# Performance work log

Hardware: AMD Instinct MI355X
Metric: run time of the kernel (lower is better)

## Reference

```python
import jax, jax.numpy as jnp
import numpy as np

N = 4096      # num nodes == input_dim
HID = 1024    # VAE hidden
LAT = 512     # VAE latent
NH = 4        # GAT heads
NHID = 64     # per-head out features
ALPHA = 0.2   # leaky-relu negative slope
NEG_INF = -9e15


def setup_inputs() -> dict:
    key = jax.random.key(0)
    ks = iter(jax.random.split(key, 32))
    def lin(shape):
        return jax.random.normal(next(ks), shape, jnp.float32) / np.float32(np.sqrt(shape[-1]))
    inp = {
        "x": jax.random.uniform(next(ks), (N,), jnp.float32),
        "eps": jax.random.normal(next(ks), (LAT,), jnp.float32),
        "adj": jax.random.uniform(next(ks), (N, N), jnp.float32) < 0.01,  # ~40 nbrs/node
        "enc_w1": lin((HID, N)), "enc_b1": jnp.zeros((HID,), jnp.float32),
        "enc_w2": lin((HID, HID)), "enc_b2": jnp.zeros((HID,), jnp.float32),
        "enc_w3": lin((LAT, HID)), "enc_b3": jnp.zeros((LAT,), jnp.float32),
        "enc_w4": lin((LAT, HID)), "enc_b4": jnp.zeros((LAT,), jnp.float32),
        "dec_w1": lin((HID, LAT)), "dec_b1": jnp.zeros((HID,), jnp.float32),
        "dec_w2": lin((HID, HID)), "dec_b2": jnp.zeros((HID,), jnp.float32),
        "dec_w3": lin((N, HID)), "dec_b3": jnp.zeros((N,), jnp.float32),
        "gat_W": lin((NH, 1, NHID)),
        "gat_a": lin((NH, 2 * NHID, 1)),
        "out_W": lin((NH * NHID, 1)),
        "out_a": lin((2, 1)),
    }
    return inp


def _linear(h, w, b):
    return h @ w.T + b


def reference(x, eps, adj, enc_w1, enc_b1, enc_w2, enc_b2, enc_w3, enc_b3,
              enc_w4, enc_b4, dec_w1, dec_b1, dec_w2, dec_b2, dec_w3, dec_b3,
              gat_W, gat_a, out_W, out_a):
    # ---- VAE encoder ----
    h = jax.nn.relu(_linear(x, enc_w1, enc_b1))
    h = jax.nn.relu(_linear(h, enc_w2, enc_b2))
    mu = _linear(h, enc_w3, enc_b3)
    logvar = _linear(h, enc_w4, enc_b4)
    # ---- reparameterize ----
    z = mu + eps * jnp.exp(0.5 * logvar)
    # ---- VAE decoder ----
    h = jax.nn.relu(_linear(z, dec_w1, dec_b1))
    h = jax.nn.relu(_linear(h, dec_w2, dec_b2))
    x_hat = jax.nn.sigmoid(_linear(h, dec_w3, dec_b3))          # [N]

    # ---- GAT (eval mode: dropout = identity) ----
    def gat_layer(xin, W, a):
        Wh = xin @ W                                             # [N, F]
        f = W.shape[1]
        e = jax.nn.leaky_relu(Wh @ a[:f] + (Wh @ a[f:]).T, ALPHA)  # [N, N]
        e = jnp.where(adj, e, NEG_INF)
        att = jax.nn.softmax(e, axis=1)
        return att @ Wh                                          # [N, F]

    xf = x_hat[:, None]                                          # [N, 1]
    heads = jax.vmap(lambda W, a: gat_layer(xf, W, a))(gat_W, gat_a)  # [NH, N, NHID]
    hcat = jnp.transpose(heads, (1, 0, 2)).reshape(N, NH * NHID)      # concat dim=1
    y_hat = jax.nn.elu(gat_layer(hcat, out_W, out_a))            # [N, 1]

    return (x_hat, y_hat, mu, logvar)
```

## Files before the change

### kernel.cpp

```cpp
#include <hip/hip_runtime.h>
#include <cstdint>
#include <cstddef>


typedef unsigned long long u64;

#define ACT_RELU 1
#define ACT_SIG  2

__device__ __forceinline__ float d4(float4 a, float4 b) {
  return a.x * b.x + a.y * b.y + a.z * b.z + a.w * b.w;
}
__device__ __forceinline__ float waveRed(float v) {
  for (int o = 32; o; o >>= 1) v += __shfl_down(v, o);
  return v;
}

__device__ __forceinline__ void csrRow(const uint4* aw, unsigned short* edges,
                                       unsigned* cnt, int r, int lane) {
  const uint4* rp = aw + (size_t)r * 1024u;
  unsigned short* er = edges + (size_t)r * 1024u;
  const u64 pm = (~0ull) >> (63 - lane);
  const u64 pmb = pm >> 1;
  unsigned total = 0;
#pragma unroll
  for (int it = 0; it < 16; ++it) {
    const uint4 v = rp[it * 64 + lane];
    const int colb = it * 256 + 4 * lane;
    u64 m;
    m = __ballot(v.x != 0u);
    if (v.x) er[min(total + (unsigned)__popcll(m & pmb), 1023u)] = (unsigned short)colb;
    total += (unsigned)__popcll(m);
    m = __ballot(v.y != 0u);
    if (v.y) er[min(total + (unsigned)__popcll(m & pmb), 1023u)] = (unsigned short)(colb + 1);
    total += (unsigned)__popcll(m);
    m = __ballot(v.z != 0u);
    if (v.z) er[min(total + (unsigned)__popcll(m & pmb), 1023u)] = (unsigned short)(colb + 2);
    total += (unsigned)__popcll(m);
    m = __ballot(v.w != 0u);
    if (v.w) er[min(total + (unsigned)__popcll(m & pmb), 1023u)] = (unsigned short)(colb + 3);
    total += (unsigned)__popcll(m);
  }
  if (lane == 0) cnt[r] = min(total, 1024u);
}

struct MegaP {
  const void* adj;
  unsigned short* edges;
  unsigned* cnt;
  const float *w1, *x, *b1;
  float* h1;
  const float *gw, *ga, *ow, *oa;
  float* consts;
};

__global__ __launch_bounds__(256) void mega_kernel(MegaP p) {
  const int tid = threadIdx.x, w = tid >> 6, lane = tid & 63;
  const int blk = blockIdx.x;
  if (blk < 1024) {
    csrRow((const uint4*)p.adj, p.edges, p.cnt, blk * 4 + w, lane);
    return;
  }
  if (blk < 2048) {
    const int r = blk - 1024;
    const float4* row = (const float4*)(p.w1 + (size_t)r * 4096u);
    const float4* x4 = (const float4*)p.x;
    float acc = 0.f;
#pragma unroll
    for (int k = 0; k < 4; ++k) {
      const int idx = tid + 256 * k;
      acc += d4(row[idx], x4[idx]);
    }
    acc = waveRed(acc);
    __shared__ float lds[4];
    if (lane == 0) lds[w] = acc;
    __syncthreads();
    if (tid == 0) {
      const float v = lds[0] + lds[1] + lds[2] + lds[3] + p.b1[r];
      p.h1[r] = v > 0.f ? v : 0.f;
    }
    return;
  }
  const int h = w, k = lane;
  const float wv = p.gw[h * 64 + k];
  float p1 = wv * p.ga[h * 128 + k];
  float p2 = wv * p.ga[h * 128 + 64 + k];
  float p3 = wv * p.ow[h * 64 + k];
  for (int off = 32; off; off >>= 1) {
    p1 += __shfl_down(p1, off);
    p2 += __shfl_down(p2, off);
    p3 += __shfl_down(p3, off);
  }
  if (k == 0) { p.consts[h] = p1; p.consts[4 + h] = p2; p.consts[8 + h] = p3; }
  if (tid == 0) { p.consts[12] = p.oa[0]; p.consts[13] = p.oa[1]; }
}

template<int ACT>
__global__ __launch_bounds__(256) void mv_kernel(const float* __restrict__ W,
    const float* __restrict__ x, const float* __restrict__ b,
    float* __restrict__ y, int C) {
  const int r = blockIdx.x;
  const float* row = W + (size_t)r * (size_t)C;
  float acc = 0.f;
  for (int c = threadIdx.x * 4; c < C; c += 256 * 4) {
    const float4 w4 = *reinterpret_cast<const float4*>(row + c);
    const float4 x4 = *reinterpret_cast<const float4*>(x + c);
    acc += d4(w4, x4);
  }
  acc = waveRed(acc);
  __shared__ float lds[4];
  if ((threadIdx.x & 63) == 0) lds[threadIdx.x >> 6] = acc;
  __syncthreads();
  if (threadIdx.x == 0) {
    float v = lds[0] + lds[1] + lds[2] + lds[3] + b[r];
    if (ACT == ACT_RELU) v = v > 0.f ? v : 0.f;
    if (ACT == ACT_SIG)  v = 1.f / (1.f + expf(-v));
    y[r] = v;
  }
}

__global__ __launch_bounds__(256) void mulv_kernel(const float* __restrict__ w3,
    const float* __restrict__ b3, const float* __restrict__ w4,
    const float* __restrict__ b4, const float* __restrict__ h2,
    float* __restrict__ mu, float* __restrict__ logvar) {
  const int r = blockIdx.x;
  const bool is_mu = r < 512;
  const int rr = is_mu ? r : r - 512;
  const float* row = (is_mu ? w3 : w4) + (size_t)rr * 1024u;
  const int c = threadIdx.x * 4;
  float acc = d4(*reinterpret_cast<const float4*>(row + c),
                 *reinterpret_cast<const float4*>(h2 + c));
  acc = waveRed(acc);
  __shared__ float lds[4];
  if ((threadIdx.x & 63) == 0) lds[threadIdx.x >> 6] = acc;
  __syncthreads();
  if (threadIdx.x == 0) {
    const float v = lds[0] + lds[1] + lds[2] + lds[3] + (is_mu ? b3[rr] : b4[rr]);
    (is_mu ? mu : logvar)[rr] = v;
  }
}

__global__ __launch_bounds__(256) void dec1_kernel(const float* __restrict__ W,
    const float* __restrict__ mu, const float* __restrict__ logvar,
    const float* __restrict__ eps, const float* __restrict__ b,
    float* __restrict__ y) {
  __shared__ float zsh[512];
  for (int k = threadIdx.x; k < 512; k += 256)
    zsh[k] = mu[k] + eps[k] * expf(0.5f * logvar[k]);
  __syncthreads();
  const int r = blockIdx.x;
  const float* row = W + (size_t)r * 512u;
  const int c = threadIdx.x * 2;
  const float2 w2 = *reinterpret_cast<const float2*>(row + c);
  float acc = w2.x * zsh[c] + w2.y * zsh[c + 1];
  acc = waveRed(acc);
  __shared__ float lds[4];
  if ((threadIdx.x & 63) == 0) lds[threadIdx.x >> 6] = acc;
  __syncthreads();
  if (threadIdx.x == 0) {
    float v = lds[0] + lds[1] + lds[2] + lds[3] + b[r];
    y[r] = v > 0.f ? v : 0.f;
  }
}

__global__ __launch_bounds__(256) void gat_heads_csr(
    const unsigned short* __restrict__ edges, const unsigned* __restrict__ cnt,
    const float* __restrict__ xh, const float* __restrict__ consts,
    float* __restrict__ wh2) {
  const int lane = threadIdx.x & 63;
  const int i = blockIdx.x * 4 + (threadIdx.x >> 6);
  const unsigned n = cnt[i];
  const float xi = xh[i];
  const float A0 = consts[0] * xi, A1 = consts[1] * xi,
              A2 = consts[2] * xi, A3 = consts[3] * xi;
  const float c20 = consts[4], c21 = consts[5], c22 = consts[6], c23 = consts[7];
  float s0 = 0, s1 = 0, s2 = 0, s3 = 0, t0 = 0, t1 = 0, t2 = 0, t3 = 0;
  const unsigned short* er = edges + (size_t)i * 1024u;
  for (unsigned j = lane; j < n; j += 64) {
    const float xj = xh[er[j]];
    float e0 = A0 + c20 * xj, e1 = A1 + c21 * xj, e2 = A2 + c22 * xj, e3 = A3 + c23 * xj;
    e0 = fmaxf(e0, 0.2f * e0); e1 = fmaxf(e1, 0.2f * e1);
    e2 = fmaxf(e2, 0.2f * e2); e3 = fmaxf(e3, 0.2f * e3);
    const float w0 = expf(e0), w1 = expf(e1), w2 = expf(e2), w3 = expf(e3);
    s0 += w0; s1 += w1; s2 += w2; s3 += w3;
    t0 += w0 * xj; t1 += w1 * xj; t2 += w2 * xj; t3 += w3 * xj;
  }
  for (int o = 1; o < 64; o <<= 1) {
    s0 += __shfl_xor(s0, o); s1 += __shfl_xor(s1, o);
    s2 += __shfl_xor(s2, o); s3 += __shfl_xor(s3, o);
    t0 += __shfl_xor(t0, o); t1 += __shfl_xor(t1, o);
    t2 += __shfl_xor(t2, o); t3 += __shfl_xor(t3, o);
  }
  float r0, r1, r2, r3;
  if (n != 0) { r0 = t0 / s0; r1 = t1 / s1; r2 = t2 / s2; r3 = t3 / s3; }
  else {
    float a = 0.f;
    for (int k = lane; k < 4096; k += 64) a += xh[k];
    for (int o = 1; o < 64; o <<= 1) a += __shfl_xor(a, o);
    r0 = r1 = r2 = r3 = a * (1.f / 4096.f);
  }
  if (lane == 0)
    wh2[i] = consts[8] * r0 + consts[9] * r1 + consts[10] * r2 + consts[11] * r3;
}

__global__ __launch_bounds__(256) void gat_out_csr(
    const unsigned short* __restrict__ edges, const unsigned* __restrict__ cnt,
    const float* __restrict__ wh2, const float* __restrict__ consts,
    float* __restrict__ yhat) {
  const int lane = threadIdx.x & 63;
  const int i = blockIdx.x * 4 + (threadIdx.x >> 6);
  const unsigned n = cnt[i];
  const float Ai = consts[12] * wh2[i];
  const float oa1 = consts[13];
  float s = 0.f, t = 0.f;
  const unsigned short* er = edges + (size_t)i * 1024u;
  for (unsigned j = lane; j < n; j += 64) {
    const float wj = wh2[er[j]];
    float e = Ai + oa1 * wj;
    e = fmaxf(e, 0.2f * e);
    const float ww = expf(e);
    s += ww; t += ww * wj;
  }
  for (int o = 1; o < 64; o <<= 1) {
    s += __shfl_xor(s, o);
    t += __shfl_xor(t, o);
  }
  float v;
  if (n != 0) v = t / s;
  else {
    float a = 0.f;
    for (int k = lane; k < 4096; k += 64) a += wh2[k];
    for (int o = 1; o < 64; o <<= 1) a += __shfl_xor(a, o);
    v = a * (1.f / 4096.f);
  }
  if (lane == 0) yhat[i] = v > 0.f ? v : expm1f(v);
}

extern "C" void kernel_launch(void* const* d_in, const int* in_sizes, int n_in,
                              void* d_out, int out_size, void* d_ws, size_t ws_size,
                              hipStream_t stream) {
  const float* x      = (const float*)d_in[0];
  const float* eps    = (const float*)d_in[1];
  const void*  adj    = d_in[2];
  const float* enc_w1 = (const float*)d_in[3];
  const float* enc_b1 = (const float*)d_in[4];
  const float* enc_w2 = (const float*)d_in[5];
  const float* enc_b2 = (const float*)d_in[6];
  const float* enc_w3 = (const float*)d_in[7];
  const float* enc_b3 = (const float*)d_in[8];
  const float* enc_w4 = (const float*)d_in[9];
  const float* enc_b4 = (const float*)d_in[10];
  const float* dec_w1 = (const float*)d_in[11];
  const float* dec_b1 = (const float*)d_in[12];
  const float* dec_w2 = (const float*)d_in[13];
  const float* dec_b2 = (const float*)d_in[14];
  const float* dec_w3 = (const float*)d_in[15];
  const float* dec_b3 = (const float*)d_in[16];
  const float* gat_W  = (const float*)d_in[17];
  const float* gat_a  = (const float*)d_in[18];
  const float* out_W  = (const float*)d_in[19];
  const float* out_a  = (const float*)d_in[20];

  float* out    = (float*)d_out;
  float* xhat   = out;
  float* yhat   = out + 4096;
  float* mu     = out + 8192;
  float* logvar = out + 8704;

  unsigned short* edges = (unsigned short*)d_ws;
  unsigned* cnt = (unsigned*)((char*)d_ws + (size_t)4096 * 1024 * 2);
  float* F      = (float*)((char*)cnt + 4096 * sizeof(unsigned));
  float* h1     = F;
  float* h2     = F + 1024;
  float* h3     = F + 2048;
  float* h4     = F + 3072;
  float* wh2    = F + 4096;
  float* consts = F + 8208;

  MegaP mp;
  mp.adj = adj; mp.edges = edges; mp.cnt = cnt;
  mp.w1 = enc_w1; mp.x = x; mp.b1 = enc_b1; mp.h1 = h1;
  mp.gw = gat_W; mp.ga = gat_a; mp.ow = out_W; mp.oa = out_a;
  mp.consts = consts;
  mega_kernel<<<2049, 256, 0, stream>>>(mp);

  mv_kernel<ACT_RELU><<<1024, 256, 0, stream>>>(enc_w2, h1, enc_b2, h2, 1024);
  mulv_kernel<<<1024, 256, 0, stream>>>(enc_w3, enc_b3, enc_w4, enc_b4, h2, mu, logvar);
  dec1_kernel<<<1024, 256, 0, stream>>>(dec_w1, mu, logvar, eps, dec_b1, h3);
  mv_kernel<ACT_RELU><<<1024, 256, 0, stream>>>(dec_w2, h3, dec_b2, h4, 1024);
  mv_kernel<ACT_SIG ><<<4096, 256, 0, stream>>>(dec_w3, h4, dec_b3, xhat, 1024);

  gat_heads_csr<<<1024, 256, 0, stream>>>(edges, cnt, xhat, consts, wh2);
  gat_out_csr<<<1024, 256, 0, stream>>>(edges, cnt, wh2, consts, yhat);
}
```

Before: 43.03 us.

## Spread adjacency CSR conversion across later matvec kernels and batch row loads

The dense-to-CSR conversion of the adjacency matrix is split so that 3328 rows are done in the first fused kernel, 256 rows in the enc_w2 matvec launch and 512 rows in the dec_w3 launch. This moves memory-bound conversion work into kernels that otherwise have spare bandwidth, shortening the critical first kernel. All 16 uint4 loads per lane are now issued before the ballot loop, raising memory-level parallelism at the cost of more registers. All conversion still finishes before the GAT kernels that read it, since they run later on the same stream.

New measurement: 45.71 us. 1.06x slower.

```diff
diff --git a/kernel.cpp b/kernel.cpp
--- a/kernel.cpp
+++ b/kernel.cpp
@@ -20,28 +20,38 @@
                                        unsigned* cnt, int r, int lane) {
   const uint4* rp = aw + (size_t)r * 1024u;
   unsigned short* er = edges + (size_t)r * 1024u;
-  const u64 pm = (~0ull) >> (63 - lane);
-  const u64 pmb = pm >> 1;
+  uint4 v[16];
+#pragma unroll
+  for (int it = 0; it < 16; ++it) v[it] = rp[it * 64 + lane];
+
+  const u64 pmb = ((~0ull) >> (63 - lane)) >> 1;
   unsigned total = 0;
 #pragma unroll
   for (int it = 0; it < 16; ++it) {
-    const uint4 v = rp[it * 64 + lane];
     const int colb = it * 256 + 4 * lane;
     u64 m;
-    m = __ballot(v.x != 0u);
-    if (v.x) er[min(total + (unsigned)__popcll(m & pmb), 1023u)] = (unsigned short)colb;
+    m = __ballot(v[it].x != 0u);
+    if (v[it].x) er[min(total + (unsigned)__popcll(m & pmb), 1023u)] = (unsigned short)colb;
     total += (unsigned)__popcll(m);
-    m = __ballot(v.y != 0u);
-    if (v.y) er[min(total + (unsigned)__popcll(m & pmb), 1023u)] = (unsigned short)(colb + 1);
+    m = __ballot(v[it].y != 0u);
+    if (v[it].y) er[min(total + (unsigned)__popcll(m & pmb), 1023u)] = (unsigned short)(colb + 1);
     total += (unsigned)__popcll(m);
-    m = __ballot(v.z != 0u);
-    if (v.z) er[min(total + (unsigned)__popcll(m & pmb), 1023u)] = (unsigned short)(colb + 2);
+    m = __ballot(v[it].z != 0u);
+    if (v[it].z) er[min(total + (unsigned)__popcll(m & pmb), 1023u)] = (unsigned short)(colb + 2);
     total += (unsigned)__popcll(m);
-    m = __ballot(v.w != 0u);
-    if (v.w) er[min(total + (unsigned)__popcll(m & pmb), 1023u)] = (unsigned short)(colb + 3);
+    m = __ballot(v[it].w != 0u);
+    if (v[it].w) er[min(total + (unsigned)__popcll(m & pmb), 1023u)] = (unsigned short)(colb + 3);
     total += (unsigned)__popcll(m);
   }
   if (lane == 0) cnt[r] = min(total, 1024u);
+}
+
+__device__ __forceinline__ bool convFirst(int CB, int convBase, const void* adj,
+                                          unsigned short* edges, unsigned* cnt) {
+  if ((int)blockIdx.x >= CB) return false;
+  const int row = convBase + blockIdx.x * 4 + (threadIdx.x >> 6);
+  csrRow((const uint4*)adj, edges, cnt, row, threadIdx.x & 63);
+  return true;
 }
 
 struct MegaP {
@@ -57,12 +67,12 @@
 __global__ __launch_bounds__(256) void mega_kernel(MegaP p) {
   const int tid = threadIdx.x, w = tid >> 6, lane = tid & 63;
   const int blk = blockIdx.x;
-  if (blk < 1024) {
+  if (blk < 832) {
     csrRow((const uint4*)p.adj, p.edges, p.cnt, blk * 4 + w, lane);
     return;
   }
-  if (blk < 2048) {
-    const int r = blk - 1024;
+  if (blk < 1856) {
+    const int r = blk - 832;
     const float4* row = (const float4*)(p.w1 + (size_t)r * 4096u);
     const float4* x4 = (const float4*)p.x;
     float acc = 0.f;
@@ -96,10 +106,13 @@
 }
 
 template<int ACT>
-__global__ __launch_bounds__(256) void mv_kernel(const float* __restrict__ W,
+__global__ __launch_bounds__(256) void mv_conv_kernel(const float* __restrict__ W,
     const float* __restrict__ x, const float* __restrict__ b,
-    float* __restrict__ y, int C) {
-  const int r = blockIdx.x;
+    float* __restrict__ y, int C, int CB, int convBase,
+    const void* __restrict__ adj, unsigned short* __restrict__ edges,
+    unsigned* __restrict__ cnt) {
+  if (CB && convFirst(CB, convBase, adj, edges, cnt)) return;
+  const int r = blockIdx.x - CB;
   const float* row = W + (size_t)r * (size_t)C;
   float acc = 0.f;
   for (int c = threadIdx.x * 4; c < C; c += 256 * 4) {
@@ -282,13 +295,16 @@
   mp.w1 = enc_w1; mp.x = x; mp.b1 = enc_b1; mp.h1 = h1;
   mp.gw = gat_W; mp.ga = gat_a; mp.ow = out_W; mp.oa = out_a;
   mp.consts = consts;
-  mega_kernel<<<2049, 256, 0, stream>>>(mp);
-
-  mv_kernel<ACT_RELU><<<1024, 256, 0, stream>>>(enc_w2, h1, enc_b2, h2, 1024);
+  mega_kernel<<<1857, 256, 0, stream>>>(mp);
+
+  mv_conv_kernel<ACT_RELU><<<64 + 1024, 256, 0, stream>>>(
+      enc_w2, h1, enc_b2, h2, 1024, 64, 3328, adj, edges, cnt);
   mulv_kernel<<<1024, 256, 0, stream>>>(enc_w3, enc_b3, enc_w4, enc_b4, h2, mu, logvar);
   dec1_kernel<<<1024, 256, 0, stream>>>(dec_w1, mu, logvar, eps, dec_b1, h3);
-  mv_kernel<ACT_RELU><<<1024, 256, 0, stream>>>(dec_w2, h3, dec_b2, h4, 1024);
-  mv_kernel<ACT_SIG ><<<4096, 256, 0, stream>>>(dec_w3, h4, dec_b3, xhat, 1024);
+  mv_conv_kernel<ACT_RELU><<<1024, 256, 0, stream>>>(
+      dec_w2, h3, dec_b2, h4, 1024, 0, 0, adj, edges, cnt);
+  mv_conv_kernel<ACT_SIG><<<128 + 4096, 256, 0, stream>>>(
+      dec_w3, h4, dec_b3, xhat, 1024, 128, 3584, adj, edges, cnt);
 
   gat_heads_csr<<<1024, 256, 0, stream>>>(edges, cnt, xhat, consts, wh2);
   gat_out_csr<<<1024, 256, 0, stream>>>(edges, cnt, wh2, consts, yhat);
```
